# Kernel optimization log

Measured on AMD Instinct MI355X. Metric: run time of the kernel, lower is better.

Reference implementation:

```python
import jax, jax.numpy as jnp
import numpy as np

INPUT_SIZE = 21
HIDDEN = 50
OUTPUT = 24
BATCH = 4096
SEQ = 336


def setup_inputs() -> dict:
    key = jax.random.key(0)
    ks = jax.random.split(key, 7)
    s_ih = 1.0 / np.sqrt(HIDDEN)
    x = jax.random.normal(ks[0], (BATCH, SEQ, INPUT_SIZE), dtype=jnp.float32)
    # PyTorch LSTM params: gate order i, f, g, o stacked along dim0
    W_ih = jax.random.uniform(ks[1], (4 * HIDDEN, INPUT_SIZE), minval=-s_ih, maxval=s_ih, dtype=jnp.float32)
    W_hh = jax.random.uniform(ks[2], (4 * HIDDEN, HIDDEN), minval=-s_ih, maxval=s_ih, dtype=jnp.float32)
    b_ih = jax.random.uniform(ks[3], (4 * HIDDEN,), minval=-s_ih, maxval=s_ih, dtype=jnp.float32)
    b_hh = jax.random.uniform(ks[4], (4 * HIDDEN,), minval=-s_ih, maxval=s_ih, dtype=jnp.float32)
    s_fc = 1.0 / np.sqrt(HIDDEN)
    W_fc = jax.random.uniform(ks[5], (OUTPUT, HIDDEN), minval=-s_fc, maxval=s_fc, dtype=jnp.float32)
    b_fc = jax.random.uniform(ks[6], (OUTPUT,), minval=-s_fc, maxval=s_fc, dtype=jnp.float32)
    return {"x": x, "W_ih": W_ih, "W_hh": W_hh, "b_ih": b_ih, "b_hh": b_hh, "W_fc": W_fc, "b_fc": b_fc}


def _lstm_last(x, W_ih, W_hh, b_ih, b_hh):
    B = x.shape[0]
    H = W_hh.shape[1]
    # Precompute input projections for all timesteps: [T, B, 4H]
    x_proj = jnp.einsum('bti,gi->tbg', x, W_ih) + (b_ih + b_hh)

    def step(carry, xp):
        h, c = carry
        gates = xp + h @ W_hh.T  # [B, 4H]
        i_g, f_g, g_g, o_g = jnp.split(gates, 4, axis=-1)
        i_g = jax.nn.sigmoid(i_g)
        f_g = jax.nn.sigmoid(f_g)
        g_g = jnp.tanh(g_g)
        o_g = jax.nn.sigmoid(o_g)
        c = f_g * c + i_g * g_g
        h = o_g * jnp.tanh(c)
        return (h, c), None

    h0 = jnp.zeros((B, H), dtype=x.dtype)
    c0 = jnp.zeros((B, H), dtype=x.dtype)
    (h_last, _), _ = jax.lax.scan(step, (h0, c0), x_proj)
    return h_last


def reference(x, W_ih, W_hh, b_ih, b_hh, W_fc, b_fc):
    h_last = _lstm_last(x, W_ih, W_hh, b_ih, b_hh)  # [B, H]
    return h_last @ W_fc.T + b_fc  # [B, OUTPUT]
```

## Files before the change

### kernel.cpp

```cpp
#include <hip/hip_runtime.h>


#define T_SEQ 336
#define I_IN  21
#define HID   50
#define O_OUT 24
#define MB    16
#define NT    512
#define TPW   2
#define CH    8
#define NCH   42
#define XELEM (CH * MB * I_IN)
#define NLD   6
#define XBUFH (CH * 4 * 16 * 8)

#define HIDX(buf, kb, n, j) ((((buf)*8 + (kb))*16 + (n))*8 + (j))
#define XIDX(s, kb, n, j)   ((((s)*4 + (kb))*16 + (n))*8 + (j))

#define K_LOG2E 1.44269504088896340736f
#define C2SCALE (2.f * K_LOG2E)

typedef _Float16 f16x8 __attribute__((ext_vector_type(8)));
typedef float    f32x4 __attribute__((ext_vector_type(4)));

#define MFMA16(A, B, C) __builtin_amdgcn_mfma_f32_16x16x32_f16((A), (B), (C), 0, 0, 0)

static __device__ __forceinline__ float frcp(float v) { return __builtin_amdgcn_rcpf(v); }
static __device__ __forceinline__ float ex2(float v)  { return __builtin_amdgcn_exp2f(v); }
static __device__ __forceinline__ float sigm2(float g) { return frcp(1.f + ex2(g)); }
static __device__ __forceinline__ float tanh2(float g) {
    return __builtin_fmaf(-2.f, frcp(1.f + ex2(g)), 1.f);
}
static __device__ __forceinline__ float tanh2s(float g) {
    return __builtin_fmaf(-2.f * C2SCALE, frcp(1.f + ex2(g)), C2SCALE);
}

#define XPROJ(sp)                                                        \
    do {                                                                 \
        const f16x8 XN = *(const f16x8*)&xC[wb + (sp) * 512 + bfo];      \
        xp[0][(sp)] = MFMA16(Xh[0], XN, biasv[0]);                       \
        xp[0][(sp)] = MFMA16(Xl[0], XN, xp[0][(sp)]);                    \
        xp[1][(sp)] = MFMA16(Xh[1], XN, biasv[1]);                       \
        xp[1][(sp)] = MFMA16(Xl[1], XN, xp[1][(sp)]);                    \
    } while (0)

__global__ __launch_bounds__(NT)
void lstm_mfma11(const float* __restrict__ x,
                 const float* __restrict__ W_ih,
                 const float* __restrict__ W_hh,
                 const float* __restrict__ b_ih,
                 const float* __restrict__ b_hh,
                 const float* __restrict__ W_fc,
                 const float* __restrict__ b_fc,
                 float* __restrict__ out)
{
    __shared__ _Float16 hbuf[2 * 8 * 16 * 8];
    __shared__ _Float16 xC[2 * XBUFH];

    const int tid  = threadIdx.x;
    const int lane = tid & 63;
    const int wv   = tid >> 6;
    const int nl   = lane & 15;
    const int q    = lane >> 4;
    const int b0   = blockIdx.x * MB;
    const int ph   = (wv ^ (wv >> 2)) & 1;

    for (int i = tid; i < 2 * 8 * 16 * 8; i += NT) hbuf[i] = (_Float16)0.f;
    for (int i = tid; i < 2 * XBUFH;      i += NT) xC[i]   = (_Float16)0.f;

    const float* px[NLD];
    int  xdst[NLD];
    bool xv[NLD];
    float sv[NLD];
    #pragma unroll
    for (int k = 0; k < NLD; ++k) {
        const int e  = tid + k * NT;
        const int i  = e % I_IN;
        const int r  = e / I_IN;
        const int b  = r & 15;
        const int sIr = r >> 4;
        const int sI = (sIr < CH) ? sIr : 0;
        xv[k]   = (e < XELEM);
        px[k]   = x + ((size_t)(b0 + b) * T_SEQ + sI) * I_IN + i;
        xdst[k] = XIDX(sI, i >> 3, b, i & 7);
        sv[k]   = px[k][0];
    }

    f16x8 Wh[TPW][2], Wl[TPW][2];
    f16x8 Xh[TPW],    Xl[TPW];
    f32x4 biasv[TPW];
    #pragma unroll
    for (int tt = 0; tt < TPW; ++tt) {
        const int t    = wv * TPW + tt;
        const int p    = t * 16 + nl;
        const int unit = p >> 2, gate = p & 3;
        const bool vr  = (unit < HID);
        const float ws = (gate == 2) ? C2SCALE : (-K_LOG2E);
        const int orig = gate * HID + unit;
        const int ub   = t * 4 + q;
        #pragma unroll
        for (int r = 0; r < 4; ++r) {
            const float bs = (r == 2) ? C2SCALE : (-K_LOG2E);
            biasv[tt][r] = (ub < HID) ? (b_ih[r * HID + ub] + b_hh[r * HID + ub]) * bs : 0.f;
        }
        #pragma unroll
        for (int kc = 0; kc < 2; ++kc) {
            #pragma unroll
            for (int j = 0; j < 8; ++j) {
                const int k = kc * 32 + q * 8 + j;
                const float w = (vr && k < HID) ? W_hh[orig * HID + k] * ws : 0.f;
                const _Float16 hi = (_Float16)w;
                Wh[tt][kc][j] = hi;
                Wl[tt][kc][j] = (_Float16)(w - (float)hi);
            }
        }
        #pragma unroll
        for (int j = 0; j < 8; ++j) {
            const int k = q * 8 + j;
            const float w = (vr && k < I_IN) ? W_ih[orig * I_IN + k] * ws : 0.f;
            const _Float16 hi = (_Float16)w;
            Xh[tt][j] = hi;
            Xl[tt][j] = (_Float16)(w - (float)hi);
        }
    }

    __syncthreads();

    #pragma unroll
    for (int k = 0; k < NLD; ++k) {
        if (xv[k]) xC[xdst[k]] = (_Float16)sv[k];
        px[k] += CH * I_IN;
    }
    __syncthreads();

    const int u0 = (wv * TPW + 0) * 4 + q;
    const int u1 = (wv * TPW + 1) * 4 + q;
    const int hwo0 = ((u0 >> 3) * 16 + nl) * 8 + (u0 & 7);
    const int hwo1 = ((u1 >> 3) * 16 + nl) * 8 + (u1 & 7);
    float cst0 = 0.f, cst1 = 0.f;

    const _Float16* hb0 = &hbuf[HIDX(0, q, nl, 0)];
    const int bfo = ((q * 16) + nl) * 8;

    f32x4 xp[TPW][CH];
    {
        const int wb = 0;
        #pragma unroll
        for (int s = 0; s < CH; ++s) XPROJ(s);
    }

    for (int c = 0; c < NCH; ++c) {
        const int  rb    = (c & 1) * XBUFH;
        const int  wb    = ((c + 1) & 1) * XBUFH;
        const bool dostg = (c + 1) < NCH;
        #pragma unroll
        for (int s = 0; s < CH; ++s) {
            __syncthreads();

            if (s == 0 && dostg) {
                #pragma unroll
                for (int k = 0; k < NLD; ++k) sv[k] = px[k][0];
            }

            const int cur = s & 1, nxt = cur ^ 1;

            const _Float16* hb = hb0 + cur * 1024;
            const f16x8 B0 = *(const f16x8*)(hb);
            const f16x8 B1 = *(const f16x8*)(hb + 512);

            if (ph) {
                if (dostg && s >= 1) XPROJ(s - 1);
                if (dostg && s == CH - 1) XPROJ(CH - 1);
            }

            __builtin_amdgcn_s_setprio(1);
            f32x4 a0 = xp[0][s];
            f32x4 a1 = xp[1][s];
            a0 = MFMA16(Wh[0][0], B0, a0);
            a1 = MFMA16(Wh[1][0], B0, a1);
            a0 = MFMA16(Wh[0][1], B1, a0);
            a1 = MFMA16(Wh[1][1], B1, a1);
            a0 = MFMA16(Wl[0][0], B0, a0);
            a1 = MFMA16(Wl[1][0], B0, a1);
            a0 = MFMA16(Wl[0][1], B1, a0);
            a1 = MFMA16(Wl[1][1], B1, a1);
            __builtin_amdgcn_s_setprio(0);

            {
                const float tg2 = tanh2s(a0[2]);
                const float cc  = __builtin_fmaf(sigm2(a0[1]), cst0,
                                                 sigm2(a0[0]) * tg2);
                cst0 = cc;
                const float h = sigm2(a0[3]) * tanh2(cc);
                hbuf[nxt * 1024 + hwo0] = (_Float16)h;
            }
            {
                const float tg2 = tanh2s(a1[2]);
                const float cc  = __builtin_fmaf(sigm2(a1[1]), cst1,
                                                 sigm2(a1[0]) * tg2);
                cst1 = cc;
                const float h = sigm2(a1[3]) * tanh2(cc);
                hbuf[nxt * 1024 + hwo1] = (_Float16)h;
            }

            if (!ph) {
                if (dostg && s >= 1) XPROJ(s - 1);
                if (dostg && s == CH - 1) XPROJ(CH - 1);
            }

            if (s == 0 && dostg) {
                #pragma unroll
                for (int k = 0; k < NLD; ++k) {
                    if (xv[k]) xC[wb + xdst[k]] = (_Float16)sv[k];
                    px[k] += CH * I_IN;
                }
            }
        }
    }

    __syncthreads();
    if (tid < MB * O_OUT) {
        const int b = tid / O_OUT, o = tid % O_OUT;
        float a = b_fc[o];
        for (int u = 0; u < HID; ++u) {
            const float hv = (float)hbuf[HIDX(0, u >> 3, b, u & 7)];
            a = __builtin_fmaf(hv, W_fc[o * HID + u], a);
        }
        out[(size_t)(b0 + b) * O_OUT + o] = a;
    }
}

extern "C" void kernel_launch(void* const* d_in, const int* in_sizes, int n_in,
                              void* d_out, int out_size, void* d_ws, size_t ws_size,
                              hipStream_t stream)
{
    const float* x    = (const float*)d_in[0];
    const float* W_ih = (const float*)d_in[1];
    const float* W_hh = (const float*)d_in[2];
    const float* b_ih = (const float*)d_in[3];
    const float* b_hh = (const float*)d_in[4];
    const float* W_fc = (const float*)d_in[5];
    const float* b_fc = (const float*)d_in[6];
    float* out = (float*)d_out;

    lstm_mfma11<<<dim3(4096 / MB), dim3(NT), 0, stream>>>(
        x, W_ih, W_hh, b_ih, b_hh, W_fc, b_fc, out);
}
```

Baseline: 318.9 us.

## Halve block size so each wave computes four gate tiles per step

Cuts the block from 8 waves to 4, with each wave owning four 16-row gate tiles instead of two. The x chunk shrinks to 4 timesteps over 84 chunks, so the staging buffer still fits. The per-wave phase split of the input projection and the s_setprio hints are removed; the projection now always runs after the activations, and the kernel requests one wave per EU. Fewer waves should make the per-timestep barrier and LDS traffic cheaper. The cost is twice the MFMA and transcendental work on each wave's serial critical path per step, and less latency hiding.

```diff
diff --git a/kernel.cpp b/kernel.cpp
--- a/kernel.cpp
+++ b/kernel.cpp
@@ -6,10 +6,10 @@
 #define HID   50
 #define O_OUT 24
 #define MB    16
-#define NT    512
-#define TPW   2
-#define CH    8
-#define NCH   42
+#define NT    256
+#define TPW   4
+#define CH    4
+#define NCH   84
 #define XELEM (CH * MB * I_IN)
 #define NLD   6
 #define XBUFH (CH * 4 * 16 * 8)
@@ -35,17 +35,21 @@
     return __builtin_fmaf(-2.f * C2SCALE, frcp(1.f + ex2(g)), C2SCALE);
 }
 
-#define XPROJ(sp)                                                        \
+#define XPROJ_ALL(sp)                                                    \
     do {                                                                 \
         const f16x8 XN = *(const f16x8*)&xC[wb + (sp) * 512 + bfo];      \
         xp[0][(sp)] = MFMA16(Xh[0], XN, biasv[0]);                       \
+        xp[1][(sp)] = MFMA16(Xh[1], XN, biasv[1]);                       \
+        xp[2][(sp)] = MFMA16(Xh[2], XN, biasv[2]);                       \
+        xp[3][(sp)] = MFMA16(Xh[3], XN, biasv[3]);                       \
         xp[0][(sp)] = MFMA16(Xl[0], XN, xp[0][(sp)]);                    \
-        xp[1][(sp)] = MFMA16(Xh[1], XN, biasv[1]);                       \
         xp[1][(sp)] = MFMA16(Xl[1], XN, xp[1][(sp)]);                    \
+        xp[2][(sp)] = MFMA16(Xl[2], XN, xp[2][(sp)]);                    \
+        xp[3][(sp)] = MFMA16(Xl[3], XN, xp[3][(sp)]);                    \
     } while (0)
 
-__global__ __launch_bounds__(NT)
-void lstm_mfma11(const float* __restrict__ x,
+__global__ __launch_bounds__(NT) __attribute__((amdgpu_waves_per_eu(1)))
+void lstm_mfma17(const float* __restrict__ x,
                  const float* __restrict__ W_ih,
                  const float* __restrict__ W_hh,
                  const float* __restrict__ b_ih,
@@ -63,7 +67,6 @@
     const int nl   = lane & 15;
     const int q    = lane >> 4;
     const int b0   = blockIdx.x * MB;
-    const int ph   = (wv ^ (wv >> 2)) & 1;
 
     for (int i = tid; i < 2 * 8 * 16 * 8; i += NT) hbuf[i] = (_Float16)0.f;
     for (int i = tid; i < 2 * XBUFH;      i += NT) xC[i]   = (_Float16)0.f;
@@ -133,11 +136,14 @@
     }
     __syncthreads();
 
-    const int u0 = (wv * TPW + 0) * 4 + q;
-    const int u1 = (wv * TPW + 1) * 4 + q;
-    const int hwo0 = ((u0 >> 3) * 16 + nl) * 8 + (u0 & 7);
-    const int hwo1 = ((u1 >> 3) * 16 + nl) * 8 + (u1 & 7);
-    float cst0 = 0.f, cst1 = 0.f;
+    int hwo[TPW];
+    float cst[TPW];
+    #pragma unroll
+    for (int tt = 0; tt < TPW; ++tt) {
+        const int u = (wv * TPW + tt) * 4 + q;
+        hwo[tt] = ((u >> 3) * 16 + nl) * 8 + (u & 7);
+        cst[tt] = 0.f;
+    }
 
     const _Float16* hb0 = &hbuf[HIDX(0, q, nl, 0)];
     const int bfo = ((q * 16) + nl) * 8;
@@ -146,13 +152,14 @@
     {
         const int wb = 0;
         #pragma unroll
-        for (int s = 0; s < CH; ++s) XPROJ(s);
+        for (int s = 0; s < CH; ++s) XPROJ_ALL(s);
     }
 
     for (int c = 0; c < NCH; ++c) {
         const int  rb    = (c & 1) * XBUFH;
         const int  wb    = ((c + 1) & 1) * XBUFH;
         const bool dostg = (c + 1) < NCH;
+        (void)rb;
         #pragma unroll
         for (int s = 0; s < CH; ++s) {
             __syncthreads();
@@ -168,45 +175,30 @@
             const f16x8 B0 = *(const f16x8*)(hb);
             const f16x8 B1 = *(const f16x8*)(hb + 512);
 
-            if (ph) {
-                if (dostg && s >= 1) XPROJ(s - 1);
-                if (dostg && s == CH - 1) XPROJ(CH - 1);
-            }
-
-            __builtin_amdgcn_s_setprio(1);
-            f32x4 a0 = xp[0][s];
-            f32x4 a1 = xp[1][s];
-            a0 = MFMA16(Wh[0][0], B0, a0);
-            a1 = MFMA16(Wh[1][0], B0, a1);
-            a0 = MFMA16(Wh[0][1], B1, a0);
-            a1 = MFMA16(Wh[1][1], B1, a1);
-            a0 = MFMA16(Wl[0][0], B0, a0);
-            a1 = MFMA16(Wl[1][0], B0, a1);
-            a0 = MFMA16(Wl[0][1], B1, a0);
-            a1 = MFMA16(Wl[1][1], B1, a1);
-            __builtin_amdgcn_s_setprio(0);
-
-            {
-                const float tg2 = tanh2s(a0[2]);
-                const float cc  = __builtin_fmaf(sigm2(a0[1]), cst0,
-                                                 sigm2(a0[0]) * tg2);
-                cst0 = cc;
-                const float h = sigm2(a0[3]) * tanh2(cc);
-                hbuf[nxt * 1024 + hwo0] = (_Float16)h;
-            }
-            {
-                const float tg2 = tanh2s(a1[2]);
-                const float cc  = __builtin_fmaf(sigm2(a1[1]), cst1,
-                                                 sigm2(a1[0]) * tg2);
-                cst1 = cc;
-                const float h = sigm2(a1[3]) * tanh2(cc);
-                hbuf[nxt * 1024 + hwo1] = (_Float16)h;
-            }
-
-            if (!ph) {
-                if (dostg && s >= 1) XPROJ(s - 1);
-                if (dostg && s == CH - 1) XPROJ(CH - 1);
-            }
+            f32x4 a[TPW];
+            #pragma unroll
+            for (int tt = 0; tt < TPW; ++tt) a[tt] = xp[tt][s];
+            #pragma unroll
+            for (int tt = 0; tt < TPW; ++tt) a[tt] = MFMA16(Wh[tt][0], B0, a[tt]);
+            #pragma unroll
+            for (int tt = 0; tt < TPW; ++tt) a[tt] = MFMA16(Wh[tt][1], B1, a[tt]);
+            #pragma unroll
+            for (int tt = 0; tt < TPW; ++tt) a[tt] = MFMA16(Wl[tt][0], B0, a[tt]);
+            #pragma unroll
+            for (int tt = 0; tt < TPW; ++tt) a[tt] = MFMA16(Wl[tt][1], B1, a[tt]);
+
+            #pragma unroll
+            for (int tt = 0; tt < TPW; ++tt) {
+                const float tg2 = tanh2s(a[tt][2]);
+                const float cc  = __builtin_fmaf(sigm2(a[tt][1]), cst[tt],
+                                                 sigm2(a[tt][0]) * tg2);
+                cst[tt] = cc;
+                const float h = sigm2(a[tt][3]) * tanh2(cc);
+                hbuf[nxt * 1024 + hwo[tt]] = (_Float16)h;
+            }
+
+            if (dostg && s >= 1) XPROJ_ALL(s - 1);
+            if (dostg && s == CH - 1) XPROJ_ALL(CH - 1);
 
             if (s == 0 && dostg) {
                 #pragma unroll
@@ -219,8 +211,8 @@
     }
 
     __syncthreads();
-    if (tid < MB * O_OUT) {
-        const int b = tid / O_OUT, o = tid % O_OUT;
+    for (int t = tid; t < MB * O_OUT; t += NT) {
+        const int b = t / O_OUT, o = t % O_OUT;
         float a = b_fc[o];
         for (int u = 0; u < HID; ++u) {
             const float hv = (float)hbuf[HIDX(0, u >> 3, b, u & 7)];
@@ -243,6 +235,6 @@
     const float* b_fc = (const float*)d_in[6];
     float* out = (float*)d_out;
 
-    lstm_mfma11<<<dim3(4096 / MB), dim3(NT), 0, stream>>>(
+    lstm_mfma17<<<dim3(4096 / MB), dim3(NT), 0, stream>>>(
         x, W_ih, W_hh, b_ih, b_hh, W_fc, b_fc, out);
 }
```

Result: slower. 353.6 us (+10.9%).
